# Performance work log

Measured on AMD Instinct MI355X. Metric: run time of the kernel, lower is better.

## Reference

```python
import jax, jax.numpy as jnp
import numpy as np

S, D, H, E = 4096, 1024, 16, 64  # seq_len, embed_dim, n_heads, head_size


def setup_inputs() -> dict:
    key = jax.random.key(0)
    ks = jax.random.split(key, 8)
    s_d = 1.0 / np.sqrt(D).astype(np.float32)
    return {
        "x": jax.random.normal(ks[0], (S, D), jnp.float32),
        # per-head Q/K/V projections (no bias), stacked over heads: [H, D, E]
        "Wk": jax.random.normal(ks[1], (H, D, E), jnp.float32) * s_d,
        "Wq": jax.random.normal(ks[2], (H, D, E), jnp.float32) * s_d,
        "Wv": jax.random.normal(ks[3], (H, D, E), jnp.float32) * s_d,
        # output projection Dense(D) with bias
        "Wo": jax.random.normal(ks[4], (H * E, D), jnp.float32) * (1.0 / np.sqrt(H * E).astype(np.float32)),
        "bo": jnp.zeros((D,), jnp.float32),
        # MLP: Dense(4D) -> gelu -> Dense(D), both with bias
        "W1": jax.random.normal(ks[5], (D, 4 * D), jnp.float32) * s_d,
        "b1": jnp.zeros((4 * D,), jnp.float32),
        "W2": jax.random.normal(ks[6], (4 * D, D), jnp.float32) * (1.0 / np.sqrt(4 * D).astype(np.float32)),
        "b2": jnp.zeros((D,), jnp.float32),
    }


def _attention(x, Wk, Wq, Wv):
    # per-head projections, vectorized over heads (original loops in Python)
    k = jnp.einsum('sd,hde->hse', x, Wk)
    q = jnp.einsum('sd,hde->hse', x, Wq)
    v = jnp.einsum('sd,hde->hse', x, Wv)
    # NOTE: original computes keys @ queries.T -> scores[i, j] = k_i . q_j
    scores = jnp.einsum('hse,hte->hst', k, q) / jnp.sqrt(jnp.float32(E))
    mask = jnp.tril(jnp.ones((x.shape[0], x.shape[0]), dtype=bool))  # [S, S]
    w = jax.nn.softmax(jnp.where(mask, scores, -jnp.inf), axis=-1)   # [H, S, S]
    out = jnp.einsum('hst,hte->hse', w, v)                            # [H, S, E]
    # concatenate heads along feature axis (head 0 first, matching the loop)
    return out.transpose(1, 0, 2).reshape(x.shape[0], -1)             # [S, H*E]


def reference(x, Wk, Wq, Wv, Wo, bo, W1, b1, W2, b2):
    x = x + _attention(x, Wk, Wq, Wv) @ Wo + bo
    h = jax.nn.gelu(x @ W1 + b1, approximate=True)  # flax default gelu (tanh approx)
    return x + h @ W2 + b2
```

## Files before the change

### kernel.cpp

```cpp
#include <hip/hip_runtime.h>

typedef __attribute__((ext_vector_type(8))) short s16x8;
typedef __attribute__((ext_vector_type(4))) short s16x4;
typedef __attribute__((ext_vector_type(4))) float f32x4;


__device__ __forceinline__ unsigned short f2bf(float f) {
    union { float f; unsigned u; } v; v.f = f;
    unsigned r = v.u + 0x7FFFu + ((v.u >> 16) & 1u);
    return (unsigned short)(r >> 16);
}

__device__ __forceinline__ unsigned cvt_pk_bf16(float lo, float hi) {
    unsigned r;
    asm("v_cvt_pk_bf16_f32 %0, %1, %2" : "=v"(r) : "v"(lo), "v"(hi));
    return r;
}

__device__ __forceinline__ float exp2_fast(float x) {
    float r;
    asm("v_exp_f32 %0, %1" : "=v"(r) : "v"(x));
    return r;
}

__device__ __forceinline__ float gelu_tanh(float x) {
    float u = 0.7978845608028654f * (x + 0.044715f * x * x * x);
    float au = fabsf(u);
    float t = 1.f - 2.f / (__expf(2.f * au) + 1.f);
    t = (u < 0.f) ? -t : t;
    return 0.5f * x * (1.f + t);
}

__device__ __forceinline__ void load_lds16(const void* g, void* l) {
    __builtin_amdgcn_global_load_lds(
        (const __attribute__((address_space(1))) void*)g,
        (__attribute__((address_space(3))) void*)l, 16, 0, 0);
}

__device__ __forceinline__ void xcd_remap(int& bx, int& by) {
    const int gx = gridDim.x;
    const int nwg = gx * gridDim.y;
    const int id = by * gx + bx;
    const int nid = (id & 7) * (nwg >> 3) + (id >> 3);
    bx = nid % gx; by = nid / gx;
}


__global__ void convert_bf16_k(const float* __restrict__ in,
                               unsigned short* __restrict__ out, int n) {
    int i = (blockIdx.x * blockDim.x + threadIdx.x) * 4;
    if (i >= n) return;
    float4 v = *(const float4*)(in + i);
    ushort4 o;
    o.x = f2bf(v.x); o.y = f2bf(v.y); o.z = f2bf(v.z); o.w = f2bf(v.w);
    *(ushort4*)(out + i) = o;
}

__global__ void transpose_k(const float* __restrict__ in,
                            unsigned short* __restrict__ out, int R, int C) {
    __shared__ float tile[32][33];
    const int b = blockIdx.z;
    const int c0 = blockIdx.x * 32, r0 = blockIdx.y * 32;
    const float* inb = in + (size_t)b * R * C;
    unsigned short* outb = out + (size_t)b * R * C;
    const int tx = threadIdx.x, ty = threadIdx.y;
    #pragma unroll
    for (int i = 0; i < 4; ++i)
        tile[ty + i*8][tx] = inb[(size_t)(r0 + ty + i*8) * C + c0 + tx];
    __syncthreads();
    #pragma unroll
    for (int i = 0; i < 4; ++i)
        outb[(size_t)(c0 + ty + i*8) * R + r0 + tx] = f2bf(tile[tx][ty + i*8]);
}

template<int EPI>
__global__ __launch_bounds__(256) void gemm_bt(
    const unsigned short* __restrict__ A,
    const unsigned short* __restrict__ BT,
    const float* __restrict__ bias,
    const float* __restrict__ resid,
    float* __restrict__ Cf,
    unsigned short* __restrict__ Cb,
    int M, int N, int K)
{
    __shared__ unsigned short As[3][128 * 32];
    __shared__ unsigned short Bs[3][128 * 32];
    const int tid = threadIdx.x;
    const int w  = tid >> 6, l = tid & 63;
    const int wr = w >> 1,  wc = w & 1;
    const int lg = l >> 4,  ll = l & 15;
    int bx = blockIdx.x, by = blockIdx.y;
    xcd_remap(bx, by);
    const int m0 = by * 128, n0 = bx * 128;

    const int srow = w * 16 + (l >> 2);
    const int scol = (((l & 3) ^ ((l >> 2) & 3))) * 8;

    f32x4 acc[4][4] = {};

    auto stage = [&](int buf, int k0) {
        #pragma unroll
        for (int i = 0; i < 2; ++i) {
            load_lds16(A  + (size_t)(m0 + srow + i*64) * K + k0 + scol,
                       (char*)As[buf] + i*4096 + w*1024);
            load_lds16(BT + (size_t)(n0 + srow + i*64) * K + k0 + scol,
                       (char*)Bs[buf] + i*4096 + w*1024);
        }
    };

    const int nsteps = K >> 5;
    stage(0, 0); stage(1, 32);
    int buf = 0;
    for (int s = 0; s < nsteps; ++s) {
        if (s + 1 < nsteps) asm volatile("s_waitcnt vmcnt(4)" ::: "memory");
        else                asm volatile("s_waitcnt vmcnt(0)" ::: "memory");
        __builtin_amdgcn_s_barrier();
        s16x8 a[4], b[4];
        #pragma unroll
        for (int m = 0; m < 4; ++m) {
            const int row = wr*64 + m*16 + ll;
            a[m] = *(const s16x8*)&As[buf][row * 32 + ((lg ^ (ll & 3)) * 8)];
        }
        #pragma unroll
        for (int n = 0; n < 4; ++n) {
            const int row = wc*64 + n*16 + ll;
            b[n] = *(const s16x8*)&Bs[buf][row * 32 + ((lg ^ (ll & 3)) * 8)];
        }
        int bnext = buf + 2; if (bnext >= 3) bnext -= 3;
        if (s + 2 < nsteps) stage(bnext, (s + 2) << 5);
        __builtin_amdgcn_s_setprio(1);
        #pragma unroll
        for (int m = 0; m < 4; ++m)
            #pragma unroll
            for (int n = 0; n < 4; ++n)
                acc[m][n] = __builtin_amdgcn_mfma_f32_16x16x32_bf16(a[m], b[n], acc[m][n], 0, 0, 0);
        __builtin_amdgcn_s_setprio(0);
        buf = (buf == 2) ? 0 : buf + 1;
    }

    #pragma unroll
    for (int m = 0; m < 4; ++m) {
        #pragma unroll
        for (int n = 0; n < 4; ++n) {
            const int col = n0 + wc*64 + n*16 + ll;
            #pragma unroll
            for (int r = 0; r < 4; ++r) {
                const int row = m0 + wr*64 + m*16 + lg*4 + r;
                float v = acc[m][n][r];
                if constexpr (EPI == 2) v = gelu_tanh(v + bias[col]);
                if constexpr (EPI == 4) v *= (col < 1024) ? 0.1803368801f : 1.0f;
                Cb[(size_t)row * N + col] = f2bf(v);
            }
        }
    }
}

template<int EPI>
__global__ __launch_bounds__(256) void gemm_bt64(
    const unsigned short* __restrict__ A,
    const unsigned short* __restrict__ BT,
    const float* __restrict__ bias,
    const float* __restrict__ resid,
    float* __restrict__ Cf,
    unsigned short* __restrict__ Cb,
    int M, int N, int K)
{
    __shared__ unsigned short As[4][128 * 32];
    __shared__ unsigned short Bs[4][64 * 32];
    const int tid = threadIdx.x;
    const int w  = tid >> 6, l = tid & 63;
    const int lg = l >> 4,  ll = l & 15;
    int bx = blockIdx.x, by = blockIdx.y;
    xcd_remap(bx, by);
    const int m0 = by * 128, n0 = bx * 64;

    const int srowA = w * 16 + (l >> 2);
    const int scolA = (((l & 3) ^ ((l >> 2) & 3))) * 8;
    const int srowB = tid >> 2;
    const int scolB = (((tid & 3) ^ ((tid >> 2) & 3))) * 8;

    f32x4 acc[2][4] = {};

    auto stage = [&](int buf, int k0) {
        #pragma unroll
        for (int i = 0; i < 2; ++i)
            load_lds16(A + (size_t)(m0 + srowA + i*64) * K + k0 + scolA,
                       (char*)As[buf] + i*4096 + w*1024);
        load_lds16(BT + (size_t)(n0 + srowB) * K + k0 + scolB,
                   (char*)Bs[buf] + w*1024);
    };

    const int nsteps = K >> 5;
    stage(0, 0); stage(1, 32); stage(2, 64);
    int buf = 0;
    for (int s = 0; s < nsteps; ++s) {
        const int rem = nsteps - 1 - s;
        if (rem >= 2)      asm volatile("s_waitcnt vmcnt(6)" ::: "memory");
        else if (rem == 1) asm volatile("s_waitcnt vmcnt(3)" ::: "memory");
        else               asm volatile("s_waitcnt vmcnt(0)" ::: "memory");
        __builtin_amdgcn_s_barrier();
        s16x8 a[2], b[4];
        #pragma unroll
        for (int m = 0; m < 2; ++m) {
            const int row = w*32 + m*16 + ll;
            a[m] = *(const s16x8*)&As[buf][row * 32 + ((lg ^ (ll & 3)) * 8)];
        }
        #pragma unroll
        for (int n = 0; n < 4; ++n) {
            const int row = n*16 + ll;
            b[n] = *(const s16x8*)&Bs[buf][row * 32 + ((lg ^ (ll & 3)) * 8)];
        }
        int bnext = buf + 3; if (bnext >= 4) bnext -= 4;
        if (s + 3 < nsteps) stage(bnext, (s + 3) << 5);
        __builtin_amdgcn_s_setprio(1);
        #pragma unroll
        for (int m = 0; m < 2; ++m)
            #pragma unroll
            for (int n = 0; n < 4; ++n)
                acc[m][n] = __builtin_amdgcn_mfma_f32_16x16x32_bf16(a[m], b[n], acc[m][n], 0, 0, 0);
        __builtin_amdgcn_s_setprio(0);
        buf = (buf + 1) & 3;
    }

    #pragma unroll
    for (int m = 0; m < 2; ++m) {
        #pragma unroll
        for (int n = 0; n < 4; ++n) {
            const int col = n0 + n*16 + ll;
            #pragma unroll
            for (int r = 0; r < 4; ++r) {
                const int row = m0 + w*32 + m*16 + lg*4 + r;
                float v = acc[m][n][r];
                if constexpr (EPI == 1 || EPI == 3) v += bias[col] + resid[(size_t)row * N + col];
                if constexpr (EPI != 3)
                    Cb[(size_t)row * N + col] = f2bf(v);
                if constexpr (EPI == 1 || EPI == 3)
                    Cf[(size_t)row * N + col] = v;
            }
        }
    }
}

__global__ __launch_bounds__(256) void attn_k(
    const unsigned short* __restrict__ Rq,
    const unsigned short* __restrict__ Ck,
    const unsigned short* __restrict__ Vt,
    unsigned short* __restrict__ Out)
{
    __shared__ unsigned short Ks[3][64 * 64];
    __shared__ unsigned short Vs[3][64 * 64];

    const int bx = blockIdx.x;
    const int h  = bx & 15;
    const int sb = 31 - (bx >> 4);
    const int TOTAL = 2*sb + 2;

    const int tid = threadIdx.x;
    const int w = tid >> 6, l = tid & 63;
    const int lg = l >> 4, ll = l & 15;

    const int gsrc  = ((l & 7) ^ (l >> 3)) * 8;
    const int kOff0 = (w*16 +     (l >> 3)) * 2048 + h*64 + gsrc;
    const int kOff1 = (w*16 + 8 + (l >> 3)) * 2048 + h*64 + gsrc;
    const int vOff0 = (h*64 + w*16 +     (l >> 3)) * 4096 + gsrc;
    const int vOff1 = (h*64 + w*16 + 8 + (l >> 3)) * 4096 + gsrc;
    const int ldsOff = w * 2048;

    int qkoff[4][2];
    #pragma unroll
    for (int jj = 0; jj < 4; ++jj) {
        const int row = jj*16 + ll, r7 = row & 7;
        qkoff[jj][0] = row*128 + ((lg)     ^ r7) * 16;
        qkoff[jj][1] = row*128 + ((4 + lg) ^ r7) * 16;
    }
    int pvoff[4][2][2];
    #pragma unroll
    for (int n = 0; n < 4; ++n) {
        const int row = n*16 + ll, r7 = row & 7;
        #pragma unroll
        for (int c = 0; c < 2; ++c) {
            const int gl = (c*4     + (lg >> 1)) ^ r7;
            const int gh = (c*4 + 2 + (lg >> 1)) ^ r7;
            pvoff[n][c][0] = row*128 + gl*16 + (lg & 1)*8;
            pvoff[n][c][1] = row*128 + gh*16 + (lg & 1)*8;
        }
    }

    auto stage = [&](int t, int buf) {
        const unsigned short* qsrc = Ck + (size_t)t * 131072;
        const unsigned short* vsrc = Vt + t * 64;
        char* kd = (char*)Ks[buf] + ldsOff;
        char* vd = (char*)Vs[buf] + ldsOff;
        load_lds16(qsrc + kOff0, kd);
        load_lds16(qsrc + kOff1, kd + 1024);
        load_lds16(vsrc + vOff0, vd);
        load_lds16(vsrc + vOff1, vd + 1024);
    };

    const int row0 = sb*128 + w*32;
    const int qgA  = row0 + ll;
    const int qgB  = row0 + 16 + ll;
    const size_t rbA = (size_t)qgA * 2048 + h*64;
    const size_t rbB = (size_t)qgB * 2048 + h*64;
    const s16x8 rA0 = *(const s16x8*)&Rq[rbA + lg*8];
    const s16x8 rA1 = *(const s16x8*)&Rq[rbA + 32 + lg*8];
    const s16x8 rB0 = *(const s16x8*)&Rq[rbB + lg*8];
    const s16x8 rB1 = *(const s16x8*)&Rq[rbB + 32 + lg*8];

    const short onebf = (short)0x3F80;
    const s16x8 ones = {onebf, onebf, onebf, onebf, onebf, onebf, onebf, onebf};

    f32x4 o[2][4] = {};
    f32x4 o4[2] = {};

    stage(0, 0); stage(1, 1);
    int buf = 0;

    for (int t = 0; t < TOTAL; ++t) {
        if (t < TOTAL-1) asm volatile("s_waitcnt vmcnt(4)" ::: "memory");
        else             asm volatile("s_waitcnt vmcnt(0)" ::: "memory");
        __builtin_amdgcn_s_barrier();
        const char* kb = (const char*)Ks[buf];
        const char* vb = (const char*)Vs[buf];
        const bool diag = (t >= 2*sb);

        f32x4 st[2][4];
        __builtin_amdgcn_s_setprio(1);
        #pragma unroll
        for (int jj = 0; jj < 4; ++jj) {
            s16x8 k0 = *(const s16x8*)(kb + qkoff[jj][0]);
            s16x8 k1 = *(const s16x8*)(kb + qkoff[jj][1]);
            f32x4 z = {0.f, 0.f, 0.f, 0.f};
            f32x4 ta = __builtin_amdgcn_mfma_f32_16x16x32_bf16(k0, rA0, z, 0, 0, 0);
            st[0][jj] = __builtin_amdgcn_mfma_f32_16x16x32_bf16(k1, rA1, ta, 0, 0, 0);
            f32x4 tb = __builtin_amdgcn_mfma_f32_16x16x32_bf16(k0, rB0, z, 0, 0, 0);
            st[1][jj] = __builtin_amdgcn_mfma_f32_16x16x32_bf16(k1, rB1, tb, 0, 0, 0);
        }
        __builtin_amdgcn_s_setprio(0);

        int bnext = buf + 2; if (bnext >= 3) bnext -= 3;
        if (t + 2 < TOTAL) stage(t + 2, bnext);

        float p[2][4][4];
        if (diag) {
            #pragma unroll
            for (int jj = 0; jj < 4; ++jj)
                #pragma unroll
                for (int r = 0; r < 4; ++r) {
                    const int jg = t*64 + jj*16 + lg*4 + r;
                    p[0][jj][r] = exp2_fast((jg > qgA) ? -3e38f : st[0][jj][r]);
                    p[1][jj][r] = exp2_fast((jg > qgB) ? -3e38f : st[1][jj][r]);
                }
        } else {
            #pragma unroll
            for (int rs = 0; rs < 2; ++rs)
                #pragma unroll
                for (int jj = 0; jj < 4; ++jj)
                    #pragma unroll
                    for (int r = 0; r < 4; ++r)
                        p[rs][jj][r] = exp2_fast(st[rs][jj][r]);
        }

        s16x8 apv[2][2];
        #pragma unroll
        for (int rs = 0; rs < 2; ++rs)
            #pragma unroll
            for (int c = 0; c < 2; ++c) {
                union { unsigned u[4]; s16x8 v; } pk;
                pk.u[0] = cvt_pk_bf16(p[rs][2*c][0],   p[rs][2*c][1]);
                pk.u[1] = cvt_pk_bf16(p[rs][2*c][2],   p[rs][2*c][3]);
                pk.u[2] = cvt_pk_bf16(p[rs][2*c+1][0], p[rs][2*c+1][1]);
                pk.u[3] = cvt_pk_bf16(p[rs][2*c+1][2], p[rs][2*c+1][3]);
                apv[rs][c] = pk.v;
            }
        __builtin_amdgcn_s_setprio(1);
        #pragma unroll
        for (int rs = 0; rs < 2; ++rs) {
            o4[rs] = __builtin_amdgcn_mfma_f32_16x16x32_bf16(apv[rs][0], ones, o4[rs], 0, 0, 0);
            o4[rs] = __builtin_amdgcn_mfma_f32_16x16x32_bf16(apv[rs][1], ones, o4[rs], 0, 0, 0);
        }
        #pragma unroll
        for (int n = 0; n < 4; ++n) {
            #pragma unroll
            for (int c = 0; c < 2; ++c) {
                s16x4 lo = *(const s16x4*)(vb + pvoff[n][c][0]);
                s16x4 hi = *(const s16x4*)(vb + pvoff[n][c][1]);
                union { s16x4 h2[2]; s16x8 v; } u;
                u.h2[0] = lo; u.h2[1] = hi;
                o[0][n] = __builtin_amdgcn_mfma_f32_16x16x32_bf16(apv[0][c], u.v, o[0][n], 0, 0, 0);
                o[1][n] = __builtin_amdgcn_mfma_f32_16x16x32_bf16(apv[1][c], u.v, o[1][n], 0, 0, 0);
            }
        }
        __builtin_amdgcn_s_setprio(0);

        buf = (buf == 2) ? 0 : buf + 1;
    }

    #pragma unroll
    for (int rs = 0; rs < 2; ++rs)
        #pragma unroll
        for (int r = 0; r < 4; ++r) {
            const float li = 1.f / o4[rs][r];
            const size_t orow = (size_t)(row0 + rs*16 + lg*4 + r) * 1024 + h * 64;
            #pragma unroll
            for (int n = 0; n < 4; ++n)
                Out[orow + n*16 + ll] = f2bf(o[rs][n][r] * li);
        }
}


extern "C" void kernel_launch(void* const* d_in, const int* in_sizes, int n_in,
                              void* d_out, int out_size, void* d_ws, size_t ws_size,
                              hipStream_t stream) {
    const float* x  = (const float*)d_in[0];
    const float* Wk = (const float*)d_in[1];
    const float* Wq = (const float*)d_in[2];
    const float* Wv = (const float*)d_in[3];
    const float* Wo = (const float*)d_in[4];
    const float* bo = (const float*)d_in[5];
    const float* W1 = (const float*)d_in[6];
    const float* b1 = (const float*)d_in[7];
    const float* W2 = (const float*)d_in[8];
    const float* b2 = (const float*)d_in[9];
    float* out = (float*)d_out;

    char* ws = (char*)d_ws;
    unsigned short* x_bf  = (unsigned short*)(ws);
    unsigned short* WqkT  = (unsigned short*)(ws + (8u  << 20));
    unsigned short* WvT   = (unsigned short*)(ws + (12u << 20));
    unsigned short* WoT   = (unsigned short*)(ws + (14u << 20));
    unsigned short* W1T   = (unsigned short*)(ws + (16u << 20));
    unsigned short* W2T   = (unsigned short*)(ws + (24u << 20));
    unsigned short* QKm   = (unsigned short*)(ws + (32u << 20));
    unsigned short* attn  = (unsigned short*)(ws + (48u << 20));
    unsigned short* Vt    = (unsigned short*)(ws + (56u << 20));
    float*          yf    = (float*)(ws + (64u << 20));
    unsigned short* y_bf  = x_bf;
    unsigned short* h_bf  = QKm;

    dim3 tb(32, 8);
    convert_bf16_k<<<4096, 256, 0, stream>>>(x, x_bf, 4096 * 1024);
    transpose_k<<<dim3(2, 32, 16),  tb, 0, stream>>>(Wq, WqkT,               1024, 64);
    transpose_k<<<dim3(2, 32, 16),  tb, 0, stream>>>(Wk, WqkT + 1024 * 1024, 1024, 64);
    transpose_k<<<dim3(2, 32, 16),  tb, 0, stream>>>(Wv, WvT, 1024, 64);
    transpose_k<<<dim3(32, 32, 1),  tb, 0, stream>>>(Wo, WoT, 1024, 1024);
    transpose_k<<<dim3(128, 32, 1), tb, 0, stream>>>(W1, W1T, 1024, 4096);
    transpose_k<<<dim3(32, 128, 1), tb, 0, stream>>>(W2, W2T, 4096, 1024);

    gemm_bt<4><<<dim3(16, 32), 256, 0, stream>>>(x_bf, WqkT, nullptr, nullptr, nullptr,
                                                 QKm, 4096, 2048, 1024);
    gemm_bt64<0><<<dim3(64, 8), 256, 0, stream>>>(WvT, x_bf, nullptr, nullptr, nullptr,
                                                  Vt, 1024, 4096, 1024);

    attn_k<<<512, 256, 0, stream>>>(QKm + 1024 , QKm , Vt, attn);

    gemm_bt64<1><<<dim3(16, 32), 256, 0, stream>>>(attn, WoT, bo, x, yf, y_bf, 4096, 1024, 1024);
    gemm_bt<2><<<dim3(32, 32),   256, 0, stream>>>(y_bf, W1T, b1, nullptr, nullptr, h_bf, 4096, 4096, 1024);
    gemm_bt64<3><<<dim3(16, 32), 256, 0, stream>>>(h_bf, W2T, b2, yf, out, nullptr, 4096, 1024, 4096);
}
```

Measured before the change: 262.3 us.

## Split causal attention key range across two blocks and combine partials

Each (head, query block) work item is now split in two: one block covers the first half of the causal key tiles and another covers the second half, doubling the grid to 1024 blocks. This is meant to improve load balance and CU occupancy across the triangular workload. Each half writes its unnormalized bf16 output and its row-sum to workspace buffers, and a new combine kernel adds the halves and normalizes. The cost is an extra kernel launch, extra memory traffic for the partials, and an extra bf16 rounding of the unnormalized partial outputs.

```diff
diff --git a/kernel.cpp b/kernel.cpp
--- a/kernel.cpp
+++ b/kernel.cpp
@@ -9,6 +9,11 @@
     union { float f; unsigned u; } v; v.f = f;
     unsigned r = v.u + 0x7FFFu + ((v.u >> 16) & 1u);
     return (unsigned short)(r >> 16);
+}
+
+__device__ __forceinline__ float bf2f(unsigned short b) {
+    union { unsigned u; float f; } v; v.u = ((unsigned)b) << 16;
+    return v.f;
 }
 
 __device__ __forceinline__ unsigned cvt_pk_bf16(float lo, float hi) {
@@ -245,15 +250,18 @@
     const unsigned short* __restrict__ Rq,
     const unsigned short* __restrict__ Ck,
     const unsigned short* __restrict__ Vt,
-    unsigned short* __restrict__ Out)
+    unsigned short* __restrict__ Ppart,
+    float* __restrict__ Lpart)
 {
     __shared__ unsigned short Ks[3][64 * 64];
     __shared__ unsigned short Vs[3][64 * 64];
 
     const int bx = blockIdx.x;
     const int h  = bx & 15;
-    const int sb = 31 - (bx >> 4);
-    const int TOTAL = 2*sb + 2;
+    const int j  = (bx >> 4) & 1;
+    const int sb = 31 - (bx >> 5);
+    const int t0 = j ? (sb + 1) : 0;
+    const int t1 = j ? (2*sb + 2) : (sb + 1);
 
     const int tid = threadIdx.x;
     const int w = tid >> 6, l = tid & 63;
@@ -313,12 +321,13 @@
     f32x4 o[2][4] = {};
     f32x4 o4[2] = {};
 
-    stage(0, 0); stage(1, 1);
+    stage(t0, 0);
+    if (t0 + 1 < t1) stage(t0 + 1, 1);
     int buf = 0;
 
-    for (int t = 0; t < TOTAL; ++t) {
-        if (t < TOTAL-1) asm volatile("s_waitcnt vmcnt(4)" ::: "memory");
-        else             asm volatile("s_waitcnt vmcnt(0)" ::: "memory");
+    for (int t = t0; t < t1; ++t) {
+        if (t < t1-1) asm volatile("s_waitcnt vmcnt(4)" ::: "memory");
+        else          asm volatile("s_waitcnt vmcnt(0)" ::: "memory");
         __builtin_amdgcn_s_barrier();
         const char* kb = (const char*)Ks[buf];
         const char* vb = (const char*)Vs[buf];
@@ -339,7 +348,7 @@
         __builtin_amdgcn_s_setprio(0);
 
         int bnext = buf + 2; if (bnext >= 3) bnext -= 3;
-        if (t + 2 < TOTAL) stage(t + 2, bnext);
+        if (t + 2 < t1) stage(t + 2, bnext);
 
         float p[2][4][4];
         if (diag) {
@@ -396,16 +405,37 @@
         buf = (buf == 2) ? 0 : buf + 1;
     }
 
+    unsigned short* Pout = Ppart + (size_t)j * 4194304;
+    float* Lout = Lpart + (size_t)j * 65536;
     #pragma unroll
     for (int rs = 0; rs < 2; ++rs)
         #pragma unroll
         for (int r = 0; r < 4; ++r) {
-            const float li = 1.f / o4[rs][r];
-            const size_t orow = (size_t)(row0 + rs*16 + lg*4 + r) * 1024 + h * 64;
+            const int row = row0 + rs*16 + lg*4 + r;
+            const size_t orow = (size_t)row * 1024 + h * 64;
             #pragma unroll
             for (int n = 0; n < 4; ++n)
-                Out[orow + n*16 + ll] = f2bf(o[rs][n][r] * li);
-        }
+                Pout[orow + n*16 + ll] = f2bf(o[rs][n][r]);
+            if (ll == 0) Lout[row * 16 + h] = o4[rs][r];
+        }
+}
+
+__global__ __launch_bounds__(256) void attn_combine_k(
+    const unsigned short* __restrict__ P,
+    const float* __restrict__ L,
+    unsigned short* __restrict__ Out)
+{
+    const int idx = (blockIdx.x * 256 + threadIdx.x) * 4;
+    const int row = idx >> 10, h = (idx & 1023) >> 6;
+    const float inv = 1.f / (L[row*16 + h] + L[65536 + row*16 + h]);
+    ushort4 a = *(const ushort4*)(P + idx);
+    ushort4 b = *(const ushort4*)(P + 4194304 + idx);
+    ushort4 o;
+    o.x = f2bf((bf2f(a.x) + bf2f(b.x)) * inv);
+    o.y = f2bf((bf2f(a.y) + bf2f(b.y)) * inv);
+    o.z = f2bf((bf2f(a.z) + bf2f(b.z)) * inv);
+    o.w = f2bf((bf2f(a.w) + bf2f(b.w)) * inv);
+    *(ushort4*)(Out + idx) = o;
 }
 
 
@@ -435,6 +465,8 @@
     unsigned short* attn  = (unsigned short*)(ws + (48u << 20));
     unsigned short* Vt    = (unsigned short*)(ws + (56u << 20));
     float*          yf    = (float*)(ws + (64u << 20));
+    float*          Lpart = (float*)ws;
+    unsigned short* Ppart = (unsigned short*)(ws + (64u << 20));
     unsigned short* y_bf  = x_bf;
     unsigned short* h_bf  = QKm;
 
@@ -452,7 +484,8 @@
     gemm_bt64<0><<<dim3(64, 8), 256, 0, stream>>>(WvT, x_bf, nullptr, nullptr, nullptr,
                                                   Vt, 1024, 4096, 1024);
 
-    attn_k<<<512, 256, 0, stream>>>(QKm + 1024 , QKm , Vt, attn);
+    attn_k<<<1024, 256, 0, stream>>>(QKm + 1024 , QKm , Vt, Ppart, Lpart);
+    attn_combine_k<<<4096, 256, 0, stream>>>(Ppart, Lpart, attn);
 
     gemm_bt64<1><<<dim3(16, 32), 256, 0, stream>>>(attn, WoT, bo, x, yf, y_bf, 4096, 1024, 1024);
     gemm_bt<2><<<dim3(32, 32),   256, 0, stream>>>(y_bf, W1T, b1, nullptr, nullptr, h_bf, 4096, 4096, 1024);
```

After: 251.8 us. 4.0% less time.
